# Optimization experiments

Hardware: AMD Instinct MI355X
Metric: run time of the kernel (lower is better)

The kernel has to match this reference:

```python
import jax, jax.numpy as jnp
import numpy as np

B, D, S = 65536, 128, 2
LAMBDA_E, LAMBDA_OD = 0.1, 0.036
GAMMA_E, GAMMA_OD = 2.0, 1.1
STEP_SIZE = 30
FLIP_IDX = 13


def setup_inputs() -> dict:
    key = jax.random.key(0)
    ks = jax.random.split(key, 16)
    return {
        "mean_t": jax.random.normal(ks[0], (B, D), jnp.float32),
        "mean_s": jax.random.normal(ks[1], (B, D), jnp.float32),
        "log_std_t": jax.random.normal(ks[2], (B, D), jnp.float32),
        "log_std_s": jax.random.normal(ks[3], (B, D), jnp.float32),
        "y_zt": jax.random.normal(ks[4], (B, 1), jnp.float32),
        "s_zt": jax.random.normal(ks[5], (B, S), jnp.float32),
        "s_zs": jax.random.normal(ks[6], (B, S), jnp.float32),
        "z1": jax.random.normal(ks[7], (B, D), jnp.float32),
        "z2": jax.random.normal(ks[8], (B, D), jnp.float32),
        "target": jax.random.uniform(ks[9], (B, 1), jnp.float32),
        "noise_pt": jax.random.normal(ks[10], (B, D), jnp.float32),
        "noise_ps": jax.random.normal(ks[11], (B, D), jnp.float32),
        "noise_et": jax.random.normal(ks[12], (B, D), jnp.float32),
        "noise_es": jax.random.normal(ks[13], (B, D), jnp.float32),
        "current_step": 10,
    }


def _bce_with_logits(logits, target):
    # stable mean BCEWithLogitsLoss
    return jnp.mean(jnp.maximum(logits, 0.0) - logits * target
                    + jnp.log1p(jnp.exp(-jnp.abs(logits))))


def _kld_batchmean(log_p_input, q_target):
    # torch KLDivLoss(log_input, target, reduction='batchmean')
    log_q = jnp.log(q_target)
    return jnp.sum(q_target * (log_q - log_p_input)) / q_target.shape[0]


def reference(mean_t, mean_s, log_std_t, log_std_s, y_zt, s_zt, s_zs,
              z1, z2, target, noise_pt, noise_ps, noise_et, noise_es,
              current_step):
    # fixed prior means: zeros with idx13=1, ones with idx13=0
    mean_1 = jnp.zeros((D,), jnp.float32).at[FLIP_IDX].set(1.0)
    mean_2 = jnp.ones((D,), jnp.float32).at[FLIP_IDX].set(0.0)

    L_t = _bce_with_logits(y_zt, target)

    # entropy loss: -sum(softmax * log_softmax) / B
    logp = jax.nn.log_softmax(s_zt, axis=1)
    Loss_e = -jnp.sum(jnp.exp(logp) * logp) / s_zt.shape[0]

    # vectorized reparameterized sampling (torch .sample() is detached)
    prior_t = mean_1[None, :] + noise_pt
    prior_s = mean_2[None, :] + noise_ps
    enc_t = jax.lax.stop_gradient(mean_t + jnp.exp(0.5 * log_std_t) * noise_et)
    enc_s = jax.lax.stop_gradient(mean_s + jnp.exp(0.5 * log_std_s) * noise_es)

    L_zt = _kld_batchmean(jax.nn.log_softmax(prior_t, axis=1),
                          jax.nn.softmax(enc_t, axis=1))
    L_zs = _kld_batchmean(jax.nn.log_softmax(prior_s, axis=1),
                          jax.nn.softmax(enc_s, axis=1))

    frac = jnp.float32(current_step) / jnp.float32(STEP_SIZE)
    lambda_e = LAMBDA_E * GAMMA_E ** frac
    lambda_od = LAMBDA_OD * GAMMA_OD ** frac
    return L_t + lambda_od * (L_zt + L_zs) + lambda_e * Loss_e
```

## Files before the change

kernel.cpp:

```cpp
#include <hip/hip_runtime.h>


#define B_SIZE 65536
#define D_SIZE 128
#define GRID   2048
#define BLOCK  256

#define L2E  1.44269504089f
#define HL2E 0.72134752045f
#define SHIFT_L2E 57.7078016356f

__device__ __forceinline__ float red8(float v) {
    v += __shfl_xor(v, 1, 64);
    v += __shfl_xor(v, 2, 64);
    v += __shfl_xor(v, 4, 64);
    return v;
}
__device__ __forceinline__ float red64(float v) {
#pragma unroll
    for (int m = 1; m <= 32; m <<= 1) v += __shfl_xor(v, m, 64);
    return v;
}

__global__ __launch_bounds__(BLOCK, 4) void ortho_main(
    const float* __restrict__ mean_t,   const float* __restrict__ mean_s,
    const float* __restrict__ log_std_t,const float* __restrict__ log_std_s,
    const float* __restrict__ y_zt,     const float* __restrict__ s_zt,
    const float* __restrict__ target,
    const float* __restrict__ noise_pt, const float* __restrict__ noise_ps,
    const float* __restrict__ noise_et, const float* __restrict__ noise_es,
    const int*  __restrict__ step,
    double* __restrict__ partial)
{
    const int lane = threadIdx.x & 63;
    const int wid  = threadIdx.x >> 6;
    const int k    = lane & 7;
    const int row  = (blockIdx.x * (BLOCK / 64) + wid) * 8 + (lane >> 3);
    const int idx  = row * D_SIZE + k * 4;

    const float frac      = (float)step[0] * (1.0f / 30.0f);
    const float lambda_e  = 0.1f   * exp2f(frac);
    const float lambda_od = 0.036f * exp2f(frac * 0.13750352374993502f);

    const float pk3 = (k == 3) ? 1.0f : 0.0f;

    float se_t = 0.f, sp_t = 0.f, sep_t = 0.f;
    float se_s = 0.f, sp_s = 0.f, sep_s = 0.f;

#define ELEM(SE, SP, SEP, MX, LX, NX, PX, PM)                         \
    {                                                                 \
        float e  = fmaf(exp2f((LX) * HL2E), (NX), (MX));              \
        float ex = exp2f(fmaf(e, L2E, -SHIFT_L2E));                   \
        float p  = (PM) + (PX);                                       \
        SE += ex;                                                     \
        SP += exp2f(p * L2E);                                         \
        SEP = fmaf(ex, e - p, SEP);                                   \
    }

#pragma unroll
    for (int j = 0; j < 4; ++j) {
        const int o = idx + j * 32;
        const float4 mt  = *(const float4*)(mean_t    + o);
        const float4 lt  = *(const float4*)(log_std_t + o);
        const float4 net = *(const float4*)(noise_et  + o);
        const float4 npt = *(const float4*)(noise_pt  + o);
        const float4 ms  = *(const float4*)(mean_s    + o);
        const float4 ls  = *(const float4*)(log_std_s + o);
        const float4 nes = *(const float4*)(noise_es  + o);
        const float4 nps = *(const float4*)(noise_ps  + o);

        const float pmt = (j == 0) ? pk3 : 0.0f;
        const float pms = (j == 0) ? 1.0f - pk3 : 1.0f;

        ELEM(se_t, sp_t, sep_t, mt.x, lt.x, net.x, npt.x, 0.0f)
        ELEM(se_t, sp_t, sep_t, mt.y, lt.y, net.y, npt.y, pmt)
        ELEM(se_t, sp_t, sep_t, mt.z, lt.z, net.z, npt.z, 0.0f)
        ELEM(se_t, sp_t, sep_t, mt.w, lt.w, net.w, npt.w, 0.0f)

        ELEM(se_s, sp_s, sep_s, ms.x, ls.x, nes.x, nps.x, 1.0f)
        ELEM(se_s, sp_s, sep_s, ms.y, ls.y, nes.y, nps.y, pms)
        ELEM(se_s, sp_s, sep_s, ms.z, ls.z, nes.z, nps.z, 1.0f)
        ELEM(se_s, sp_s, sep_s, ms.w, ls.w, nes.w, nps.w, 1.0f)
    }
#undef ELEM

    se_t = red8(se_t); sp_t = red8(sp_t); sep_t = red8(sep_t);
    se_s = red8(se_s); sp_s = red8(sp_s); sep_s = red8(sep_s);

    float comb = 0.0f;
    if (k == 0) {
        const float kl_t = sep_t / se_t - 40.0f + (__logf(sp_t) - __logf(se_t));
        const float kl_s = sep_s / se_s - 40.0f + (__logf(sp_s) - __logf(se_s));
        comb = lambda_od * (kl_t + kl_s);
    }

    if (threadIdx.x < 32) {
        const int b = blockIdx.x * 32 + threadIdx.x;
        const float y = y_zt[b];
        const float t = target[b];
        const float bce = fmaxf(y, 0.f) - y * t + __logf(1.0f + exp2f(-fabsf(y) * L2E));
        const float2 s = *(const float2*)(s_zt + 2 * (size_t)b);
        const float m   = fmaxf(s.x, s.y);
        const float lse = m + __logf(exp2f((s.x - m) * L2E) + exp2f((s.y - m) * L2E));
        const float l0 = s.x - lse, l1 = s.y - lse;
        const float ent = -(exp2f(l0 * L2E) * l0 + exp2f(l1 * L2E) * l1);
        comb += bce + lambda_e * ent;
    }

    comb = red64(comb);
    __shared__ float sm[BLOCK / 64];
    if (lane == 0) sm[wid] = comb;
    __syncthreads();
    if (threadIdx.x == 0) {
        float t0 = 0.f;
#pragma unroll
        for (int w = 0; w < BLOCK / 64; ++w) t0 += sm[w];
        partial[blockIdx.x] = (double)t0;
    }
}

__global__ void ortho_final(const double* __restrict__ partial,
                            float* __restrict__ out)
{
    double s = 0.0;
    for (int i = threadIdx.x; i < GRID; i += BLOCK) s += partial[i];
#pragma unroll
    for (int m = 1; m <= 32; m <<= 1) s += __shfl_xor(s, m, 64);
    __shared__ double sm[BLOCK / 64];
    const int lane = threadIdx.x & 63;
    const int wid  = threadIdx.x >> 6;
    if (lane == 0) sm[wid] = s;
    __syncthreads();
    if (threadIdx.x == 0) {
        double tot = 0.0;
#pragma unroll
        for (int w = 0; w < BLOCK / 64; ++w) tot += sm[w];
        out[0] = (float)(tot / (double)B_SIZE);
    }
}

extern "C" void kernel_launch(void* const* d_in, const int* in_sizes, int n_in,
                              void* d_out, int out_size, void* d_ws, size_t ws_size,
                              hipStream_t stream) {
    const float* mean_t    = (const float*)d_in[0];
    const float* mean_s    = (const float*)d_in[1];
    const float* log_std_t = (const float*)d_in[2];
    const float* log_std_s = (const float*)d_in[3];
    const float* y_zt      = (const float*)d_in[4];
    const float* s_zt      = (const float*)d_in[5];
    const float* target    = (const float*)d_in[9];
    const float* noise_pt  = (const float*)d_in[10];
    const float* noise_ps  = (const float*)d_in[11];
    const float* noise_et  = (const float*)d_in[12];
    const float* noise_es  = (const float*)d_in[13];
    const int*   step      = (const int*)d_in[14];

    double* partial = (double*)d_ws;
    float*  out     = (float*)d_out;

    hipLaunchKernelGGL(ortho_main, dim3(GRID), dim3(BLOCK), 0, stream,
                       mean_t, mean_s, log_std_t, log_std_s,
                       y_zt, s_zt, target,
                       noise_pt, noise_ps, noise_et, noise_es, step, partial);
    hipLaunchKernelGGL(ortho_final, dim3(1), dim3(BLOCK), 0, stream, partial, out);
}
```

Baseline: 304.7 us.

## Split t/s streams across blocks with double-buffered nontemporal loads

Each block now handles only the t or the s stream, picked by block parity, and each wave covers 32 rows instead of 8, so the grid shrinks from 2048 to 1024 blocks. Loads use nontemporal vector loads in a software-pipelined, double-buffered loop that prefetches the next row chunk while computing the current one, with a reduction per row every four iterations. The goal is fewer loads in flight per iteration, better prefetch overlap and less cache pollution on a bandwidth-bound streaming reduction. The cost is fewer total waves, which may hurt latency hiding, and the BCE/entropy part now covers 64 rows per block.

After: 275.0 us. 1.11x faster.

```diff
diff --git a/kernel.cpp b/kernel.cpp
--- a/kernel.cpp
+++ b/kernel.cpp
@@ -3,12 +3,18 @@
 
 #define B_SIZE 65536
 #define D_SIZE 128
-#define GRID   2048
+#define GRID   1024
 #define BLOCK  256
 
 #define L2E  1.44269504089f
 #define HL2E 0.72134752045f
 #define SHIFT_L2E 57.7078016356f
+
+typedef float vf4 __attribute__((ext_vector_type(4)));
+
+__device__ __forceinline__ vf4 ntload(const float* p) {
+    return __builtin_nontemporal_load((const vf4*)p);
+}
 
 __device__ __forceinline__ float red8(float v) {
     v += __shfl_xor(v, 1, 64);
@@ -35,17 +41,27 @@
     const int lane = threadIdx.x & 63;
     const int wid  = threadIdx.x >> 6;
     const int k    = lane & 7;
-    const int row  = (blockIdx.x * (BLOCK / 64) + wid) * 8 + (lane >> 3);
-    const int idx  = row * D_SIZE + k * 4;
+    const int sub  = lane >> 3;
+
+    const int sflag = blockIdx.x & 1;
+    const int wave  = (blockIdx.x >> 1) * (BLOCK / 64) + wid;
+
+    const float* __restrict__ Am = sflag ? mean_s    : mean_t;
+    const float* __restrict__ Al = sflag ? log_std_s : log_std_t;
+    const float* __restrict__ An = sflag ? noise_es  : noise_et;
+    const float* __restrict__ Ap = sflag ? noise_ps  : noise_pt;
+
+    const float pk3    = (k == 3) ? 1.0f : 0.0f;
+    const float pm_def = sflag ? 1.0f : 0.0f;
+    const float pm_y0  = sflag ? 1.0f - pk3 : pk3;
+
+    const int off = (wave * 32 + sub) * D_SIZE + k * 4;
 
     const float frac      = (float)step[0] * (1.0f / 30.0f);
     const float lambda_e  = 0.1f   * exp2f(frac);
     const float lambda_od = 0.036f * exp2f(frac * 0.13750352374993502f);
 
-    const float pk3 = (k == 3) ? 1.0f : 0.0f;
-
-    float se_t = 0.f, sp_t = 0.f, sep_t = 0.f;
-    float se_s = 0.f, sp_s = 0.f, sep_s = 0.f;
+    float comb = 0.0f;
 
 #define ELEM(SE, SP, SEP, MX, LX, NX, PX, PM)                         \
     {                                                                 \
@@ -57,45 +73,38 @@
         SEP = fmaf(ex, e - p, SEP);                                   \
     }
 
+    vf4 bm[2], bl[2], bn[2], bp[2];
+    bm[0] = ntload(Am + off); bl[0] = ntload(Al + off);
+    bn[0] = ntload(An + off); bp[0] = ntload(Ap + off);
+
+    float se = 0.f, sp = 0.f, sep = 0.f;
 #pragma unroll
-    for (int j = 0; j < 4; ++j) {
-        const int o = idx + j * 32;
-        const float4 mt  = *(const float4*)(mean_t    + o);
-        const float4 lt  = *(const float4*)(log_std_t + o);
-        const float4 net = *(const float4*)(noise_et  + o);
-        const float4 npt = *(const float4*)(noise_pt  + o);
-        const float4 ms  = *(const float4*)(mean_s    + o);
-        const float4 ls  = *(const float4*)(log_std_s + o);
-        const float4 nes = *(const float4*)(noise_es  + o);
-        const float4 nps = *(const float4*)(noise_ps  + o);
-
-        const float pmt = (j == 0) ? pk3 : 0.0f;
-        const float pms = (j == 0) ? 1.0f - pk3 : 1.0f;
-
-        ELEM(se_t, sp_t, sep_t, mt.x, lt.x, net.x, npt.x, 0.0f)
-        ELEM(se_t, sp_t, sep_t, mt.y, lt.y, net.y, npt.y, pmt)
-        ELEM(se_t, sp_t, sep_t, mt.z, lt.z, net.z, npt.z, 0.0f)
-        ELEM(se_t, sp_t, sep_t, mt.w, lt.w, net.w, npt.w, 0.0f)
-
-        ELEM(se_s, sp_s, sep_s, ms.x, ls.x, nes.x, nps.x, 1.0f)
-        ELEM(se_s, sp_s, sep_s, ms.y, ls.y, nes.y, nps.y, pms)
-        ELEM(se_s, sp_s, sep_s, ms.z, ls.z, nes.z, nps.z, 1.0f)
-        ELEM(se_s, sp_s, sep_s, ms.w, ls.w, nes.w, nps.w, 1.0f)
+    for (int it = 0; it < 16; ++it) {
+        const int j   = it & 3;
+        const int cur = it & 1, nxt = cur ^ 1;
+        if (it < 15) {
+            const int it2 = it + 1;
+            const int o2  = off + (it2 >> 2) * (8 * D_SIZE) + (it2 & 3) * 32;
+            bm[nxt] = ntload(Am + o2); bl[nxt] = ntload(Al + o2);
+            bn[nxt] = ntload(An + o2); bp[nxt] = ntload(Ap + o2);
+        }
+        if (j == 0) { se = 0.f; sp = 0.f; sep = 0.f; }
+        const float pmy = (j == 0) ? pm_y0 : pm_def;
+        ELEM(se, sp, sep, bm[cur].x, bl[cur].x, bn[cur].x, bp[cur].x, pm_def)
+        ELEM(se, sp, sep, bm[cur].y, bl[cur].y, bn[cur].y, bp[cur].y, pmy)
+        ELEM(se, sp, sep, bm[cur].z, bl[cur].z, bn[cur].z, bp[cur].z, pm_def)
+        ELEM(se, sp, sep, bm[cur].w, bl[cur].w, bn[cur].w, bp[cur].w, pm_def)
+        if (j == 3) {
+            float rse = red8(se), rsp = red8(sp), rsep = red8(sep);
+            if (k == 0)
+                comb += rsep / rse - 40.0f + (__logf(rsp) - __logf(rse));
+        }
     }
 #undef ELEM
+    comb *= lambda_od;
 
-    se_t = red8(se_t); sp_t = red8(sp_t); sep_t = red8(sep_t);
-    se_s = red8(se_s); sp_s = red8(sp_s); sep_s = red8(sep_s);
-
-    float comb = 0.0f;
-    if (k == 0) {
-        const float kl_t = sep_t / se_t - 40.0f + (__logf(sp_t) - __logf(se_t));
-        const float kl_s = sep_s / se_s - 40.0f + (__logf(sp_s) - __logf(se_s));
-        comb = lambda_od * (kl_t + kl_s);
-    }
-
-    if (threadIdx.x < 32) {
-        const int b = blockIdx.x * 32 + threadIdx.x;
+    if (threadIdx.x < 64) {
+        const int b = blockIdx.x * 64 + threadIdx.x;
         const float y = y_zt[b];
         const float t = target[b];
         const float bce = fmaxf(y, 0.f) - y * t + __logf(1.0f + exp2f(-fabsf(y) * L2E));
```
